# Kernel tuning notes

Hardware: AMD Instinct MI355X
Metric: run time of the kernel (lower is better)

Reference implementation:

```python
import jax, jax.numpy as jnp
import numpy as np

H_GRID = 256
W_GRID = 256


def setup_inputs() -> dict:
    key = jax.random.key(0)
    k1, k2, k3, k4 = jax.random.split(key, 4)
    B, N = 8, 32768
    in_ch, out_ch = 14, 64
    xyzp = jax.random.uniform(k1, (B, N, 4), dtype=jnp.float32)  # x,y,t,p all in [0,1]
    features = jax.random.normal(k2, (B, N, in_ch), dtype=jnp.float32)
    W = jax.random.normal(k3, (9, in_ch + 2, out_ch), dtype=jnp.float32) * 0.05  # 3x3 kernel taps
    bias = jax.random.normal(k4, (out_ch,), dtype=jnp.float32) * 0.05
    return {"xyzp": xyzp, "features": features, "W": W, "bias": bias}


def reference(xyzp, features, W, bias):
    # SparseConv: voxelize points onto an (h+1)x(w+1) grid with 'mean' pooling of
    # duplicates, run a 3x3 submanifold sparse conv (inactive sites contribute 0),
    # then map results back to point order.
    h, w = H_GRID, W_GRID
    Hd, Wd = h + 1, w + 1  # round(y*h) in [0,h]
    B, N, _ = xyzp.shape
    Cin = features.shape[-1] + 2

    # yxb coordinates (note: column order [y, x] as in _get_yxb)
    y = jnp.clip(jnp.round(xyzp[..., 1] * h), 0, h).astype(jnp.int32).reshape(-1)
    x = jnp.clip(jnp.round(xyzp[..., 0] * w), 0, w).astype(jnp.int32).reshape(-1)
    b = jnp.repeat(jnp.arange(B, dtype=jnp.int32), N)

    # per-point features: [pos, neg, features]
    p = xyzp[..., 3:4]
    f = jnp.concatenate([p, 1.0 - p, features], axis=-1).reshape(B * N, Cin)

    # InputLayer mode='mean': scatter-mean duplicate coordinates into voxels
    flat = (b * Hd + y) * Wd + x  # [B*N]
    S = B * Hd * Wd
    vox_sum = jax.ops.segment_sum(f, flat, num_segments=S)            # [S, Cin]
    cnt = jax.ops.segment_sum(jnp.ones((B * N, 1), f.dtype), flat, num_segments=S)
    vox = vox_sum / jnp.maximum(cnt, 1.0)  # inactive voxels stay exactly 0

    # Submanifold 3x3 conv evaluated at each point's (active) site.
    offs = jnp.array([(dy, dx) for dy in (-1, 0, 1) for dx in (-1, 0, 1)], jnp.int32)  # [9,2]
    ny = y[:, None] + offs[None, :, 0]  # [B*N, 9]
    nx = x[:, None] + offs[None, :, 1]
    valid = (ny >= 0) & (ny < Hd) & (nx >= 0) & (nx < Wd)
    nidx = (b[:, None] * Hd + jnp.clip(ny, 0, Hd - 1)) * Wd + jnp.clip(nx, 0, Wd - 1)
    nb = vox[nidx] * valid[..., None].astype(f.dtype)  # [B*N, 9, Cin]; inactive -> 0

    out = jnp.einsum('pkc,kcd->pd', nb, W) + bias  # [B*N, out_ch]
    return out.reshape(B, N, -1)
```

## Files before the change

kernel.cpp:

```cpp
#include <hip/hip_runtime.h>

#define HD 257
#define WD 257
#define NB (8 * HD)
#define NCHUNK 32
#define CAPC 32
#define BPTS 1024
#define COUT 64
#define LROW 17
#define GPTS 64

typedef unsigned int uint;
typedef unsigned short ushort;
typedef short short8 __attribute__((ext_vector_type(8)));
typedef float f32x4 __attribute__((ext_vector_type(4)));

__device__ __forceinline__ uint pack_bf16(float a, float b) {
    uint ua = __float_as_uint(a), ub = __float_as_uint(b);
    ua += 0x7fffu + ((ua >> 16) & 1u);
    ub += 0x7fffu + ((ub >> 16) & 1u);
    return (ua >> 16) | (ub & 0xffff0000u);
}
__device__ __forceinline__ unsigned short bf16_1(float a) {
    uint ua = __float_as_uint(a);
    ua += 0x7fffu + ((ua >> 16) & 1u);
    return (unsigned short)(ua >> 16);
}

__global__ __launch_bounds__(256) void bin_kernel(
    const float* __restrict__ xyzp,
    uint* __restrict__ cnt2,
    ushort* __restrict__ pidx,
    int N) {
    __shared__ uint hist[HD];
    const int tid = threadIdx.x;
    const int chunk = blockIdx.x;
    const int b = blockIdx.y;
    const int p0 = chunk * BPTS;
    for (int i = tid; i < HD; i += 256) hist[i] = 0u;
    __syncthreads();

    const float4* xp = reinterpret_cast<const float4*>(xyzp) + (size_t)b * N;
    uint rec[BPTS / 256];
#pragma unroll
    for (int k = 0; k < BPTS / 256; ++k) {
        int i = p0 + tid + k * 256;
        float4 v = xp[i];
        int y = (int)fminf(fmaxf(rintf(v.y * 256.0f), 0.0f), 256.0f);
        uint r = atomicAdd(&hist[y], 1u);
        rec[k] = (uint)y | (r << 9);
    }
    __syncthreads();

    for (int y = tid; y < HD; y += 256)
        cnt2[(size_t)(b * HD + y) * NCHUNK + chunk] = min(hist[y], (uint)CAPC);

#pragma unroll
    for (int k = 0; k < BPTS / 256; ++k) {
        int y = rec[k] & 511;
        uint r = rec[k] >> 9;
        if (r < CAPC)
            pidx[((size_t)(b * HD + y) * NCHUNK + chunk) * CAPC + r] =
                (ushort)(p0 + tid + k * 256);
    }
}

__global__ __launch_bounds__(256) void accum_kernel(
    const uint* __restrict__ cnt2,
    const ushort* __restrict__ pidx,
    const float* __restrict__ xyzp,
    const float* __restrict__ feat,
    uint* __restrict__ voxn,
    int logN) {
    __shared__ float l[WD * LROW];
    __shared__ uint pc[NCHUNK];
    const int tid = threadIdx.x;
    const int bucket = blockIdx.x;
    const int b = bucket / HD;
    for (int i = tid; i < WD * LROW; i += 256) l[i] = 0.0f;
    if (tid < NCHUNK)
        pc[tid] = cnt2[(size_t)bucket * NCHUNK + tid];
    __syncthreads();

#pragma unroll
    for (int s = 0; s < NCHUNK * CAPC; s += 256) {
        int slot = s + tid;
        int c = slot >> 5;
        int j = slot & (CAPC - 1);
        if ((uint)j < pc[c]) {
            uint lp = pidx[((size_t)bucket * NCHUNK + c) * CAPC + j];
            int p = (b << logN) + (int)lp;
            float4 v = reinterpret_cast<const float4*>(xyzp)[p];
            int x = (int)fminf(fmaxf(rintf(v.x * 256.0f), 0.0f), 256.0f);
            float* cell = l + x * LROW;
            atomicAdd(&cell[0], v.w);
            atomicAdd(&cell[1], 1.0f - v.w);
            const float2* f2 = reinterpret_cast<const float2*>(feat + (size_t)p * 14);
#pragma unroll
            for (int jj = 0; jj < 7; ++jj) {
                float2 fv = f2[jj];
                atomicAdd(&cell[2 + 2 * jj], fv.x);
                atomicAdd(&cell[3 + 2 * jj], fv.y);
            }
        }
    }
    __syncthreads();

    for (int x = tid; x < WD; x += 256) {
        const float* c = l + x * LROW;
        float inv = __builtin_amdgcn_rcpf(fmaxf(c[0] + c[1], 1.0f));
        uint o[8];
#pragma unroll
        for (int j = 0; j < 8; ++j)
            o[j] = pack_bf16(c[2 * j] * inv, c[2 * j + 1] * inv);
        uint4* op = reinterpret_cast<uint4*>(voxn + ((size_t)bucket * WD + x) * 8);
        op[0] = make_uint4(o[0], o[1], o[2], o[3]);
        op[1] = make_uint4(o[4], o[5], o[6], o[7]);
    }
}

__global__ __launch_bounds__(256) void gather_mfma_kernel(
    const float* __restrict__ xyzp,
    const uint* __restrict__ voxn,
    const float* __restrict__ W,
    const float* __restrict__ bias,
    float* __restrict__ out, int logN) {
    __shared__ __align__(16) char sA[GPTS * 336];
    __shared__ int sCell[GPTS];
    __shared__ uint sYX[GPTS];

    const int tid = threadIdx.x;
    const int lane = tid & 63;
    const int w = tid >> 6;
    const int p0 = blockIdx.x * GPTS;
    const int hi = lane >> 4;
    const int lo = lane & 15;

    if (tid < GPTS) {
        float4 v = reinterpret_cast<const float4*>(xyzp)[p0 + tid];
        int y = (int)fminf(fmaxf(rintf(v.y * 256.0f), 0.0f), 256.0f);
        int x = (int)fminf(fmaxf(rintf(v.x * 256.0f), 0.0f), 256.0f);
        int b = (p0 + tid) >> logN;
        sCell[tid] = (b * HD + y) * WD + x;
        sYX[tid] = ((uint)y << 16) | (uint)x;
    }

    short8 bfrag[5];
    float bv = bias[w * 16 + lo];
#pragma unroll
    for (int s = 0; s < 5; ++s) {
        int kbase = s * 32 + hi * 8;
        short8 f;
#pragma unroll
        for (int j = 0; j < 8; ++j) {
            int k = kbase + j;
            float wv = (k < 144) ? W[(size_t)k * 64 + w * 16 + lo] : 0.0f;
            f[j] = (short)bf16_1(wv);
        }
        bfrag[s] = f;
    }
    __syncthreads();

    for (int idx = tid; idx < GPTS * 18; idx += 256) {
        int i = idx / 18;
        int r = idx - i * 18;
        int seg = r / 6;
        int h = r - seg * 6;
        int kx = h >> 1;
        int half = h & 1;
        uint yx = sYX[i];
        int y = (int)(yx >> 16), x = (int)(yx & 0xffffu);
        int ny = y + seg - 1, nx = x + kx - 1;
        uint4 val = make_uint4(0, 0, 0, 0);
        if ((uint)ny <= 256u && (uint)nx <= 256u) {
            size_t ncell = (size_t)sCell[i] + (size_t)((seg - 1) * WD + (kx - 1));
            val = *reinterpret_cast<const uint4*>(
                reinterpret_cast<const char*>(voxn) + ncell * 32 + (size_t)half * 16);
        }
        *reinterpret_cast<uint4*>(sA + i * 336 + (seg * 3 + kx) * 32 + half * 16) = val;
    }
    if (tid < GPTS * 2) {
        int i = tid >> 1, h = tid & 1;
        *reinterpret_cast<uint4*>(sA + i * 336 + 288 + h * 16) = make_uint4(0, 0, 0, 0);
    }
    __syncthreads();

    f32x4 acc[4];
#pragma unroll
    for (int mt = 0; mt < 4; ++mt) acc[mt] = (f32x4){bv, bv, bv, bv};

#pragma unroll
    for (int mt = 0; mt < 4; ++mt) {
        const char* abase = sA + (mt * 16 + lo) * 336 + hi * 16;
#pragma unroll
        for (int s = 0; s < 5; ++s) {
            short8 a = *reinterpret_cast<const short8*>(abase + s * 64);
            acc[mt] = __builtin_amdgcn_mfma_f32_16x16x32_bf16(a, bfrag[s], acc[mt], 0, 0, 0);
        }
    }

#pragma unroll
    for (int mt = 0; mt < 4; ++mt)
#pragma unroll
        for (int r = 0; r < 4; ++r) {
            int row = mt * 16 + hi * 4 + r;
            __builtin_nontemporal_store(acc[mt][r],
                                        &out[(size_t)(p0 + row) * 64 + w * 16 + lo]);
        }
}

extern "C" void kernel_launch(void* const* d_in, const int* in_sizes, int n_in,
                              void* d_out, int out_size, void* d_ws, size_t ws_size,
                              hipStream_t stream) {
    const float* xyzp = (const float*)d_in[0];
    const float* feat = (const float*)d_in[1];
    const float* W    = (const float*)d_in[2];
    const float* bias = (const float*)d_in[3];
    float* out = (float*)d_out;

    const int BN = in_sizes[0] / 4;
    const int B = 8;
    const int N = BN / B;
    int logN = 0;
    while ((1 << logN) < N) ++logN;

    uint* cnt2 = (uint*)d_ws;
    ushort* pidx = (ushort*)((char*)cnt2 + (size_t)NB * NCHUNK * 4);
    uint* voxn = (uint*)((char*)pidx + (size_t)NB * NCHUNK * CAPC * 2);
    (void)ws_size;

    dim3 bgrid(NCHUNK, B);
    bin_kernel<<<bgrid, 256, 0, stream>>>(xyzp, cnt2, pidx, N);
    accum_kernel<<<NB, 256, 0, stream>>>(cnt2, pidx, xyzp, feat, voxn, logN);
    gather_mfma_kernel<<<BN / GPTS, 256, 0, stream>>>(xyzp, voxn, W, bias, out, logN);
}
```

Before: 67.32 us.

## Process gather points in row-sorted order for neighbor locality

The accumulation kernel now also writes a compacted list of (y,x,point id) entries, grouped by row bucket, using a global atomic counter to allocate per-bucket ranges. The gather/MFMA kernel reads points from this sorted list instead of in original order, so each block's 3x3 neighbor reads hit nearby voxel rows and cache better. Output is scattered back to the original point index. This adds an 8-byte-per-point write and read plus scattered output stores. The design also relies on the per-chunk capacity never overflowing, because otherwise some output rows would never be written.

```diff
diff --git a/kernel.cpp b/kernel.cpp
--- a/kernel.cpp
+++ b/kernel.cpp
@@ -31,12 +31,14 @@
     const float* __restrict__ xyzp,
     uint* __restrict__ cnt2,
     ushort* __restrict__ pidx,
+    uint* __restrict__ gcnt,
     int N) {
     __shared__ uint hist[HD];
     const int tid = threadIdx.x;
     const int chunk = blockIdx.x;
     const int b = blockIdx.y;
     const int p0 = chunk * BPTS;
+    if (chunk == 0 && b == 0 && tid == 0) *gcnt = 0u;
     for (int i = tid; i < HD; i += 256) hist[i] = 0u;
     __syncthreads();
 
@@ -71,15 +73,27 @@
     const float* __restrict__ xyzp,
     const float* __restrict__ feat,
     uint* __restrict__ voxn,
+    uint2* __restrict__ sorted2,
+    uint* __restrict__ gcnt,
     int logN) {
     __shared__ float l[WD * LROW];
     __shared__ uint pc[NCHUNK];
+    __shared__ uint cbase[NCHUNK];
+    __shared__ uint sBase;
     const int tid = threadIdx.x;
     const int bucket = blockIdx.x;
     const int b = bucket / HD;
+    const int yb = bucket - b * HD;
     for (int i = tid; i < WD * LROW; i += 256) l[i] = 0.0f;
     if (tid < NCHUNK)
         pc[tid] = cnt2[(size_t)bucket * NCHUNK + tid];
+    __syncthreads();
+    if (tid == 0) {
+        uint a = 0;
+#pragma unroll
+        for (int c = 0; c < NCHUNK; ++c) { cbase[c] = a; a += pc[c]; }
+        sBase = atomicAdd(gcnt, a);
+    }
     __syncthreads();
 
 #pragma unroll
@@ -92,6 +106,8 @@
             int p = (b << logN) + (int)lp;
             float4 v = reinterpret_cast<const float4*>(xyzp)[p];
             int x = (int)fminf(fmaxf(rintf(v.x * 256.0f), 0.0f), 256.0f);
+            sorted2[sBase + cbase[c] + j] =
+                make_uint2(((uint)yb << 16) | (uint)x, (uint)p);
             float* cell = l + x * LROW;
             atomicAdd(&cell[0], v.w);
             atomicAdd(&cell[1], 1.0f - v.w);
@@ -120,7 +136,7 @@
 }
 
 __global__ __launch_bounds__(256) void gather_mfma_kernel(
-    const float* __restrict__ xyzp,
+    const uint2* __restrict__ sorted2,
     const uint* __restrict__ voxn,
     const float* __restrict__ W,
     const float* __restrict__ bias,
@@ -128,6 +144,7 @@
     __shared__ __align__(16) char sA[GPTS * 336];
     __shared__ int sCell[GPTS];
     __shared__ uint sYX[GPTS];
+    __shared__ uint sPid[GPTS];
 
     const int tid = threadIdx.x;
     const int lane = tid & 63;
@@ -137,12 +154,13 @@
     const int lo = lane & 15;
 
     if (tid < GPTS) {
-        float4 v = reinterpret_cast<const float4*>(xyzp)[p0 + tid];
-        int y = (int)fminf(fmaxf(rintf(v.y * 256.0f), 0.0f), 256.0f);
-        int x = (int)fminf(fmaxf(rintf(v.x * 256.0f), 0.0f), 256.0f);
-        int b = (p0 + tid) >> logN;
+        uint2 e = sorted2[p0 + tid];
+        int y = (int)(e.x >> 16), x = (int)(e.x & 0xffffu);
+        uint pid = e.y;
+        int b = (int)(pid >> logN);
         sCell[tid] = (b * HD + y) * WD + x;
-        sYX[tid] = ((uint)y << 16) | (uint)x;
+        sYX[tid] = e.x;
+        sPid[tid] = pid;
     }
 
     short8 bfrag[5];
@@ -204,8 +222,9 @@
 #pragma unroll
         for (int r = 0; r < 4; ++r) {
             int row = mt * 16 + hi * 4 + r;
+            uint pid = sPid[row];
             __builtin_nontemporal_store(acc[mt][r],
-                                        &out[(size_t)(p0 + row) * 64 + w * 16 + lo]);
+                                        &out[(size_t)pid * 64 + w * 16 + lo]);
         }
 }
 
@@ -227,10 +246,12 @@
     uint* cnt2 = (uint*)d_ws;
     ushort* pidx = (ushort*)((char*)cnt2 + (size_t)NB * NCHUNK * 4);
     uint* voxn = (uint*)((char*)pidx + (size_t)NB * NCHUNK * CAPC * 2);
+    uint2* sorted2 = (uint2*)((char*)voxn + (size_t)(B * HD * WD) * 32);
+    uint* gcnt = (uint*)((char*)sorted2 + (size_t)BN * 8);
     (void)ws_size;
 
     dim3 bgrid(NCHUNK, B);
-    bin_kernel<<<bgrid, 256, 0, stream>>>(xyzp, cnt2, pidx, N);
-    accum_kernel<<<NB, 256, 0, stream>>>(cnt2, pidx, xyzp, feat, voxn, logN);
-    gather_mfma_kernel<<<BN / GPTS, 256, 0, stream>>>(xyzp, voxn, W, bias, out, logN);
-}
+    bin_kernel<<<bgrid, 256, 0, stream>>>(xyzp, cnt2, pidx, gcnt, N);
+    accum_kernel<<<NB, 256, 0, stream>>>(cnt2, pidx, xyzp, feat, voxn, sorted2, gcnt, logN);
+    gather_mfma_kernel<<<BN / GPTS, 256, 0, stream>>>(sorted2, voxn, W, bias, out, logN);
+}
```

Result: slower. 87.34 us (+29.7%).
